# Kernel tuning notes

Measured on AMD Instinct MI355X. Metric: run time of the kernel, lower is better.

## Reference

```python
import jax, jax.numpy as jnp
import numpy as np


def _nn_sq_dists(query, ref):
    # query: [B, N, 3], ref: [B, M, 3]
    # squared distance via ||q||^2 + ||r||^2 - 2 q.r, min over ref points
    q2 = jnp.sum(query * query, axis=-1)            # [B, N]
    r2 = jnp.sum(ref * ref, axis=-1)                # [B, M]
    cross = jnp.einsum('bnc,bmc->bnm', query, ref)  # [B, N, M]
    d = q2[:, :, None] + r2[:, None, :] - 2.0 * cross
    d = jnp.maximum(d, 0.0)  # clamp numerical negatives (true distances >= 0)
    return jnp.min(d, axis=-1)                      # [B, N] 1-NN squared dists


def setup_inputs() -> dict:
    key = jax.random.key(0)
    k1, k2 = jax.random.split(key)
    B, C, N = 4, 3, 8192
    pc2 = jax.random.normal(k1, (B, C, N), dtype=jnp.float32)
    pc1_warped = jax.random.normal(k2, (B, C, N), dtype=jnp.float32)
    return {"pc2": pc2, "pc1_warped": pc1_warped}


def reference(pc2, pc1_warped):
    # pos1 = target['pc2'], pos2 = output['pc1_warped'], both [B, 3, N]
    pos1 = jnp.transpose(pc2, (0, 2, 1))         # [B, N, 3]
    pos2 = jnp.transpose(pc1_warped, (0, 2, 1))  # [B, N, 3]
    # pointutils.knn(1, pos1, pos2): for each pos1 point, nearest in pos2.
    nn_d = _nn_sq_dists(pos1, pos2)              # [B, N]
    per_batch = jnp.sum(nn_d, axis=1)            # sum over dim 1
    loss = per_batch.mean() + per_batch.mean()
    return loss
```

## Files before the change

kernel.cpp:

```cpp
#include <hip/hip_runtime.h>


#define NPTS 8192
#define NB   4
#define RRN  8
#define QGN  16
#define BT   512

typedef float f32x16 __attribute__((ext_vector_type(16)));
typedef short bf16x8 __attribute__((ext_vector_type(8)));

static __device__ __forceinline__ unsigned int f2bf(float f) {
    unsigned int u = __float_as_uint(f);
    u += 0x7FFF + ((u >> 16) & 1);
    return u >> 16;
}
static __device__ __forceinline__ float bf2f(unsigned int s) {
    return __uint_as_float(s << 16);
}

static __device__ __forceinline__ bf16x8 make_bfrag(float x, float y, float z,
                                                    int lane)
{
    unsigned xh = f2bf(x), yh = f2bf(y), zh = f2bf(z);
    unsigned xl = f2bf(x - bf2f(xh));
    unsigned yl = f2bf(y - bf2f(yh));
    unsigned zl = f2bf(z - bf2f(zh));
    uint4 bu = (lane < 32)
        ? make_uint4(xh | (xh << 16), xl | (yh << 16),
                     yh | (yl << 16), zh | (zh << 16))
        : make_uint4(zl | (0x3F80u << 16), 0x3F80u, 0u, 0u);
    return __builtin_bit_cast(bf16x8, bu);
}

static __device__ __forceinline__ void proc_chunk(
    uint4 av, bf16x8 bq0, bf16x8 bq1, const f32x16& zero,
    float& rma0, float& rma1, float& rma2, float& rma3,
    float& rmb0, float& rmb1, float& rmb2, float& rmb3)
{
    bf16x8 aa = __builtin_bit_cast(bf16x8, av);
    f32x16 d0 = __builtin_amdgcn_mfma_f32_32x32x16_bf16(aa, bq0, zero, 0, 0, 0);
    f32x16 d1 = __builtin_amdgcn_mfma_f32_32x32x16_bf16(aa, bq1, zero, 0, 0, 0);
    rma0 = fmaxf(rma0, fmaxf(d0[0],  d0[1]));
    rma0 = fmaxf(rma0, fmaxf(d0[2],  d0[3]));
    rma1 = fmaxf(rma1, fmaxf(d0[4],  d0[5]));
    rma1 = fmaxf(rma1, fmaxf(d0[6],  d0[7]));
    rma2 = fmaxf(rma2, fmaxf(d0[8],  d0[9]));
    rma2 = fmaxf(rma2, fmaxf(d0[10], d0[11]));
    rma3 = fmaxf(rma3, fmaxf(d0[12], d0[13]));
    rma3 = fmaxf(rma3, fmaxf(d0[14], d0[15]));
    rmb0 = fmaxf(rmb0, fmaxf(d1[0],  d1[1]));
    rmb0 = fmaxf(rmb0, fmaxf(d1[2],  d1[3]));
    rmb1 = fmaxf(rmb1, fmaxf(d1[4],  d1[5]));
    rmb1 = fmaxf(rmb1, fmaxf(d1[6],  d1[7]));
    rmb2 = fmaxf(rmb2, fmaxf(d1[8],  d1[9]));
    rmb2 = fmaxf(rmb2, fmaxf(d1[10], d1[11]));
    rmb3 = fmaxf(rmb3, fmaxf(d1[12], d1[13]));
    rmb3 = fmaxf(rmb3, fmaxf(d1[14], d1[15]));
}

__global__ __launch_bounds__(BT, 4) void chamfer_main(
    const float* __restrict__ pc2,
    const float* __restrict__ pc1w,
    float* __restrict__ partial,
    float* __restrict__ out)
{
    __shared__ uint4 slds[32 * 64];
    const int tid  = threadIdx.x;
    const int wave = tid >> 6;
    const int lane = tid & 63;
    const int b    = blockIdx.z;
    const int rr   = blockIdx.y;
    const int qg   = blockIdx.x;

    if (qg == 0 && rr == 0 && b == 0 && tid == 0) out[0] = 0.0f;

    const float* refb = pc1w + b * 3 * NPTS + rr * 1024;
#pragma unroll
    for (int j = 0; j < 2; ++j) {
        int i = tid + j * BT;
        float x = refb[i], y = refb[NPTS + i], z = refb[2 * NPTS + i];
        unsigned xh = f2bf(x), yh = f2bf(y), zh = f2bf(z);
        unsigned xl = f2bf(x - bf2f(xh));
        unsigned yl = f2bf(y - bf2f(yh));
        unsigned zl = f2bf(z - bf2f(zh));
        float h = -0.5f * (x * x + y * y + z * z);
        unsigned hh = f2bf(h);
        unsigned hl = f2bf(h - bf2f(hh));
        int c = i >> 5, l32 = i & 31;
        slds[c * 64 + l32] =
            make_uint4(xh | (xl << 16), xh | (yh << 16),
                       yl | (yh << 16), zh | (zl << 16));
        slds[c * 64 + 32 + l32] = make_uint4(zh | (hh << 16), hl, 0u, 0u);
    }

    const int qc0 = qg * 16 + wave * 2;
    const float* qb = pc2 + b * 3 * NPTS;
    const int qn0 = qc0 * 32 + (lane & 31);
    const int qn1 = qn0 + 32;
    float x0 = qb[qn0], y0 = qb[NPTS + qn0], z0 = qb[2 * NPTS + qn0];
    float x1 = qb[qn1], y1 = qb[NPTS + qn1], z1 = qb[2 * NPTS + qn1];
    bf16x8 bq0 = make_bfrag(x0, y0, z0, lane);
    bf16x8 bq1 = make_bfrag(x1, y1, z1, lane);

    f32x16 zero;
#pragma unroll
    for (int i = 0; i < 16; ++i) zero[i] = 0.0f;

    float rma0 = -3e38f, rma1 = -3e38f, rma2 = -3e38f, rma3 = -3e38f;
    float rmb0 = -3e38f, rmb1 = -3e38f, rmb2 = -3e38f, rmb3 = -3e38f;

    __syncthreads();

    uint4 av = slds[lane];
#pragma unroll 4
    for (int c = 0; c < 32; ++c) {
        uint4 acur = av;
        if (c + 1 < 32)
            av = slds[(c + 1) * 64 + lane];
        proc_chunk(acur, bq0, bq1, zero, rma0, rma1, rma2, rma3,
                   rmb0, rmb1, rmb2, rmb3);
    }

    float rma = fmaxf(fmaxf(rma0, rma1), fmaxf(rma2, rma3));
    float rmb = fmaxf(fmaxf(rmb0, rmb1), fmaxf(rmb2, rmb3));
    rma = fmaxf(rma, __shfl_xor(rma, 32, 64));
    rmb = fmaxf(rmb, __shfl_xor(rmb, 32, 64));
    float* pb = partial + ((size_t)b * RRN + rr) * NPTS + qc0 * 32;
    if (lane < 32) {
        pb[lane]      = rma;
        pb[32 + lane] = rmb;
    }
}

__global__ __launch_bounds__(512) void chamfer_reduce(
    const float* __restrict__ pc2,
    const float* __restrict__ partial,
    float* __restrict__ out)
{
    const int g = blockIdx.x * 512 + threadIdx.x;
    const int b = g >> 13, n = g & 8191;
    float smax = -3e38f;
#pragma unroll
    for (int c = 0; c < RRN; ++c)
        smax = fmaxf(smax, partial[((size_t)b * RRN + c) * NPTS + n]);

    const float* qb = pc2 + b * 3 * NPTS;
    float qx = qb[n], qy = qb[NPTS + n], qz = qb[2 * NPTS + n];
    float q2 = qx * qx + qy * qy + qz * qz;
    float d = fmaxf(q2 - 2.0f * smax, 0.0f);

#pragma unroll
    for (int off = 32; off > 0; off >>= 1)
        d += __shfl_down(d, off, 64);

    __shared__ float wsum[8];
    const int lane = threadIdx.x & 63;
    const int wid  = threadIdx.x >> 6;
    if (lane == 0) wsum[wid] = d;
    __syncthreads();
    if (threadIdx.x == 0) {
        float s = 0.0f;
#pragma unroll
        for (int w = 0; w < 8; ++w) s += wsum[w];
        atomicAdd(out, s * (2.0f / NB));
    }
}

extern "C" void kernel_launch(void* const* d_in, const int* in_sizes, int n_in,
                              void* d_out, int out_size, void* d_ws, size_t ws_size,
                              hipStream_t stream) {
    const float* pc2  = (const float*)d_in[0];
    const float* pc1w = (const float*)d_in[1];
    float* out = (float*)d_out;
    float* partial = (float*)d_ws;

    dim3 g1(QGN, RRN, NB);
    chamfer_main<<<g1, BT, 0, stream>>>(pc2, pc1w, partial, out);
    chamfer_reduce<<<NB * NPTS / 512, 512, 0, stream>>>(pc2, partial, out);
}
```

Before: 73.51 us.

## Fuse reduce kernel into main via last-block atomic counter

Removes the separate reduction kernel launch. Each block bumps a per-(batch, query-group) counter after writing its partial maxima, and the last of the RRN blocks for that group does the final max, distance and sum reduction, then atomically adds into the output. The output and the counters are zeroed with two hipMemsetAsync calls before the launch. This trades one kernel launch and its dependency for two memset operations, extra threadfences, and a serial tail in the last-arriving blocks.

```diff
diff --git a/kernel.cpp b/kernel.cpp
--- a/kernel.cpp
+++ b/kernel.cpp
@@ -59,10 +59,11 @@
     rmb3 = fmaxf(rmb3, fmaxf(d1[14], d1[15]));
 }
 
-__global__ __launch_bounds__(BT, 4) void chamfer_main(
+__global__ __launch_bounds__(BT, 4) void chamfer_fused(
     const float* __restrict__ pc2,
     const float* __restrict__ pc1w,
     float* __restrict__ partial,
+    int*   __restrict__ counter,
     float* __restrict__ out)
 {
     __shared__ uint4 slds[32 * 64];
@@ -72,8 +73,6 @@
     const int b    = blockIdx.z;
     const int rr   = blockIdx.y;
     const int qg   = blockIdx.x;
-
-    if (qg == 0 && rr == 0 && b == 0 && tid == 0) out[0] = 0.0f;
 
     const float* refb = pc1w + b * 3 * NPTS + rr * 1024;
 #pragma unroll
@@ -131,35 +130,34 @@
         pb[lane]      = rma;
         pb[32 + lane] = rmb;
     }
-}
 
-__global__ __launch_bounds__(512) void chamfer_reduce(
-    const float* __restrict__ pc2,
-    const float* __restrict__ partial,
-    float* __restrict__ out)
-{
-    const int g = blockIdx.x * 512 + threadIdx.x;
-    const int b = g >> 13, n = g & 8191;
+    __threadfence();
+    __shared__ int amlast;
+    if (tid == 0) {
+        int prev = atomicAdd(&counter[b * QGN + qg], 1);
+        amlast = (prev == RRN - 1);
+    }
+    __syncthreads();
+    if (!amlast) return;
+    __threadfence();
+
+    const int n = qg * 512 + tid;
     float smax = -3e38f;
 #pragma unroll
     for (int c = 0; c < RRN; ++c)
         smax = fmaxf(smax, partial[((size_t)b * RRN + c) * NPTS + n]);
 
-    const float* qb = pc2 + b * 3 * NPTS;
     float qx = qb[n], qy = qb[NPTS + n], qz = qb[2 * NPTS + n];
-    float q2 = qx * qx + qy * qy + qz * qz;
-    float d = fmaxf(q2 - 2.0f * smax, 0.0f);
+    float d = fmaxf(qx * qx + qy * qy + qz * qz - 2.0f * smax, 0.0f);
 
 #pragma unroll
     for (int off = 32; off > 0; off >>= 1)
         d += __shfl_down(d, off, 64);
 
     __shared__ float wsum[8];
-    const int lane = threadIdx.x & 63;
-    const int wid  = threadIdx.x >> 6;
-    if (lane == 0) wsum[wid] = d;
+    if (lane == 0) wsum[wave] = d;
     __syncthreads();
-    if (threadIdx.x == 0) {
+    if (tid == 0) {
         float s = 0.0f;
 #pragma unroll
         for (int w = 0; w < 8; ++w) s += wsum[w];
@@ -174,8 +172,11 @@
     const float* pc1w = (const float*)d_in[1];
     float* out = (float*)d_out;
     float* partial = (float*)d_ws;
+    int*   counter = (int*)((char*)d_ws + (2u << 20));
+
+    hipMemsetAsync(out, 0, sizeof(float), stream);
+    hipMemsetAsync(counter, 0, NB * QGN * sizeof(int), stream);
 
     dim3 g1(QGN, RRN, NB);
-    chamfer_main<<<g1, BT, 0, stream>>>(pc2, pc1w, partial, out);
-    chamfer_reduce<<<NB * NPTS / 512, 512, 0, stream>>>(pc2, partial, out);
+    chamfer_fused<<<g1, BT, 0, stream>>>(pc2, pc1w, partial, counter, out);
 }
```

Measured after the change: 138.4 us. 88.3% more time.
